# Optimization experiments

Measured on AMD Instinct MI355X. Metric: run time of the kernel, lower is better.

## Reference

```python
import jax, jax.numpy as jnp
import numpy as np

D = 128
NP_, NU_, NS_ = 50000, 100000, 20000
E_UP, E_PS, E_SU = 400000, 300000, 300000
# node type ids: 0=proxy, 1=user, 2=server
# edge types: (src_type, dst_type): (user->proxy), (proxy->server), (server->user)
EDGE_TYPES = [(1, 0), (0, 2), (2, 1)]


def _edge_index(key, e, n_src, n_dst):
    k0, k1 = jax.random.split(key)
    return jnp.stack([
        jax.random.randint(k0, (e,), 0, n_src),
        jax.random.randint(k1, (e,), 0, n_dst),
    ]).astype(jnp.int64)


def setup_inputs() -> dict:
    key = jax.random.key(0)
    ks = jax.random.split(key, 16)
    s = 0.05
    return {
        "x_proxy": jax.random.normal(ks[0], (NP_, 20), jnp.float32),
        "x_user": jax.random.normal(ks[1], (NU_, 20), jnp.float32),
        "x_server": jax.random.normal(ks[2], (NS_, 20), jnp.float32),
        "node_id_proxy": jnp.arange(NP_, dtype=jnp.int64),
        "node_id_user": jnp.arange(NU_, dtype=jnp.int64),
        "node_id_server": jnp.arange(NS_, dtype=jnp.int64),
        "ei_user_proxy": _edge_index(ks[3], E_UP, NU_, NP_),
        "ei_proxy_server": _edge_index(ks[4], E_PS, NP_, NS_),
        "ei_server_user": _edge_index(ks[5], E_SU, NS_, NU_),
        "lin_w": jax.random.normal(ks[6], (3, 20, D), jnp.float32) * s,
        "lin_b": jnp.zeros((3, D), jnp.float32),
        "emb_proxy": jax.random.normal(ks[7], (NP_, D), jnp.float32) * s,
        "emb_user": jax.random.normal(ks[8], (NU_, D), jnp.float32) * s,
        "emb_server": jax.random.normal(ks[9], (NS_, D), jnp.float32) * s,
        "qkv_w": jax.random.normal(ks[10], (2, 3, 3, D, D), jnp.float32) * s,
        "qkv_b": jnp.zeros((2, 3, 3, D), jnp.float32),
        "W_edge": jax.random.normal(ks[11], (2, 3, D, D), jnp.float32) * s,
    }


def _hetero_attention_layer(xs, qkv_w, qkv_b, W_e, edges):
    # xs: list of [N_t, D] node features per node type
    # edges: list of (src_type, dst_type, edge_index[2, E])
    outs = [jnp.zeros_like(x) for x in xs]
    scale = 1.0 / jnp.sqrt(jnp.asarray(D, jnp.float32))
    for et, (src_t, dst_t, ei) in enumerate(edges):
        q = xs[src_t] @ qkv_w[src_t, 0] + qkv_b[src_t, 0]   # [Ns, D]
        k = xs[dst_t] @ qkv_w[dst_t, 1] + qkv_b[dst_t, 1]   # [Nd, D]
        v = xs[src_t] @ qkv_w[src_t, 2] + qkv_b[src_t, 2]   # [Ns, D]
        src, dst = ei[0], ei[1]
        # per-edge score: q[src] @ W @ k[dst] / sqrt(D)
        s = jnp.einsum("ed,df,ef->e", q[src], W_e[et], k[dst]) * scale
        s = jax.nn.leaky_relu(s)
        n_dst = xs[dst_t].shape[0]
        # softmax normalized over edges sharing a destination node
        m = jax.ops.segment_max(s, dst, num_segments=n_dst)
        ex = jnp.exp(s - m[dst])
        den = jax.ops.segment_sum(ex, dst, num_segments=n_dst)
        alpha = ex / den[dst]                                # [E]
        msg = alpha[:, None] * v[src]                        # [E, D]
        outs[dst_t] = outs[dst_t] + jax.ops.segment_sum(msg, dst, num_segments=n_dst)
    return outs


def reference(x_proxy, x_user, x_server, node_id_proxy, node_id_user, node_id_server,
              ei_user_proxy, ei_proxy_server, ei_server_user,
              lin_w, lin_b, emb_proxy, emb_user, emb_server, qkv_w, qkv_b, W_edge):
    xs = [
        x_proxy @ lin_w[0] + lin_b[0] + emb_proxy[node_id_proxy],
        x_user @ lin_w[1] + lin_b[1] + emb_user[node_id_user],
        x_server @ lin_w[2] + lin_b[2] + emb_server[node_id_server],
    ]
    edges = [
        (EDGE_TYPES[0][0], EDGE_TYPES[0][1], ei_user_proxy),
        (EDGE_TYPES[1][0], EDGE_TYPES[1][1], ei_proxy_server),
        (EDGE_TYPES[2][0], EDGE_TYPES[2][1], ei_server_user),
    ]
    xs = _hetero_attention_layer(xs, qkv_w[0], qkv_b[0], W_edge[0], edges)
    xs = [jax.nn.relu(x) for x in xs]
    xs = _hetero_attention_layer(xs, qkv_w[1], qkv_b[1], W_edge[1], edges)
    # concatenate per-type outputs [proxy; user; server] -> [(NP+NU+NS), D]
    return jnp.concatenate(xs, axis=0)
```

## Files before the change

### kernel.cpp

```cpp
#include <hip/hip_runtime.h>

#define NP 50000
#define NU 100000
#define NS 20000
#define NTOT 170000
#define E0 400000
#define E1 300000
#define E2 300000

typedef _Float16 f16;
typedef __attribute__((ext_vector_type(8))) _Float16 half8;
typedef __attribute__((ext_vector_type(4))) _Float16 half4;
typedef __attribute__((ext_vector_type(4))) float f32x4;
typedef unsigned int uint32;

__global__ __launch_bounds__(256) void k_init_all(
    const float* __restrict__ xp, const float* __restrict__ xu,
    const float* __restrict__ xs, const int* __restrict__ nidp,
    const int* __restrict__ nidu, const int* __restrict__ nids,
    const float* __restrict__ lin_w, const float* __restrict__ lin_b,
    const float* __restrict__ embp, const float* __restrict__ embu,
    const float* __restrict__ embs, f16* __restrict__ xb) {
  int tid = threadIdx.x;
  int node = blockIdx.x * 8 + (tid >> 5);
  int dg = tid & 31;
  int t, local;
  const float* x;
  const int* nid;
  const float* emb;
  if (node < NP) { t = 0; local = node; x = xp; nid = nidp; emb = embp; }
  else if (node < NP + NU) { t = 1; local = node - NP; x = xu; nid = nidu; emb = embu; }
  else { t = 2; local = node - NP - NU; x = xs; nid = nids; emb = embs; }
  const float* lw = lin_w + t * 20 * 128;
  int d = dg * 4;
  float xv = (dg < 20) ? x[local * 20 + dg] : 0.f;
  float4 s = *(const float4*)&emb[(size_t)nid[local] * 128 + d];
  float4 b = *(const float4*)&lin_b[t * 128 + d];
  s.x += b.x; s.y += b.y; s.z += b.z; s.w += b.w;
#pragma unroll
  for (int j = 0; j < 20; ++j) {
    float xj = __shfl(xv, j, 32);
    float4 w = *(const float4*)&lw[j * 128 + d];
    s.x += xj * w.x; s.y += xj * w.y; s.z += xj * w.z; s.w += xj * w.w;
  }
  half4 o;
  o[0] = (f16)s.x; o[1] = (f16)s.y; o[2] = (f16)s.z; o[3] = (f16)s.w;
  *(half4*)(xb + (size_t)node * 128 + d) = o;
}

__global__ __launch_bounds__(128) void k_keff(const float* __restrict__ qkv_w,
                                              const float* __restrict__ qkv_b,
                                              const float* __restrict__ W_edge,
                                              float* __restrict__ Keff,
                                              float* __restrict__ bkeff) {
  int y = blockIdx.y;
  int l = y / 3, t = y - l * 3;
  int et = (t == 0) ? 0 : (t == 1) ? 2 : 1;
  const float* Wk = qkv_w + (size_t)(y * 3 + 1) * 16384;
  const float* bk = qkv_b + (size_t)(y * 3 + 1) * 128;
  const float* We = W_edge + (size_t)(l * 3 + et) * 16384;
  float* Ko = Keff + (size_t)y * 16384;
  float* bo = bkeff + (size_t)y * 128;

  __shared__ float Wes[128][65];
  int c = blockIdx.x, tid = threadIdx.x;
  float s = 0.f, tb = 0.f;
  for (int f0 = 0; f0 < 128; f0 += 64) {
    __syncthreads();
    int fr = tid & 63, r0 = tid >> 6;
    for (int it = 0; it < 64; ++it) {
      int row = it * 2 + r0;
      Wes[row][fr] = We[row * 128 + f0 + fr];
    }
    __syncthreads();
#pragma unroll 16
    for (int fp = 0; fp < 64; ++fp) s += Wk[c * 128 + f0 + fp] * Wes[tid][fp];
    if (c == 0) {
      for (int fp = 0; fp < 64; ++fp) tb += bk[f0 + fp] * Wes[tid][fp];
    }
  }
  Ko[c * 128 + tid] = s;
  if (c == 0) bo[tid] = tb;
}

__global__ __launch_bounds__(256) void k_splitw18(const float* __restrict__ qkv_w,
                                                  const float* __restrict__ Keff6,
                                                  f16* __restrict__ hi,
                                                  f16* __restrict__ lo) {
  int slot = blockIdx.y;
  int y = slot / 3, r = slot - y * 3;
  const float* src = (r == 1) ? (Keff6 + (size_t)y * 16384)
                              : (qkv_w + (size_t)(y * 3 + ((r == 0) ? 0 : 2)) * 16384);
  f16* h = hi + (size_t)slot * 16384;
  f16* l = lo + (size_t)slot * 16384;
  int idx = blockIdx.x * 256 + threadIdx.x;
  int n = idx >> 7, c = idx & 127;
  float f = src[c * 128 + n];
  f16 hb = (f16)f;
  h[idx] = hb;
  l[idx] = (f16)(f - (float)hb);
}

#define GB0 782
#define GB1 1563
#define GB2 313
__global__ __launch_bounds__(256, 4) void k_gemm3(
    const f16* __restrict__ Xin,
    const f16* __restrict__ WtHi, const f16* __restrict__ WtLo,
    const float* __restrict__ qkv_b, const float* __restrict__ bkeff6,
    f16* __restrict__ QV, f16* __restrict__ Kb, int l) {
  __shared__ f16 As[64 * 128];
  __shared__ f16 Ys[64 * 128];
  int bid = blockIdx.x;
  int t, row0, M, moff;
  if (bid < GB0) { t = 0; row0 = bid * 64; M = NP; moff = 0; }
  else if (bid < GB0 + GB1) { t = 1; row0 = (bid - GB0) * 64; M = NU; moff = NP; }
  else { t = 2; row0 = (bid - GB0 - GB1) * 64; M = NS; moff = NP + NU; }
  int y = l * 3 + t;
  const f16* A = Xin + (size_t)moff * 128;
  const f16* Whi = WtHi + (size_t)y * 3 * 16384;
  const f16* Wlo = WtLo + (size_t)y * 3 * 16384;

  int tid = threadIdx.x;
  int wave = tid >> 6, lane = tid & 63;
  int colw = wave * 32;
  int lrow = lane & 15, kgrp = lane >> 4;

#pragma unroll
  for (int i = 0; i < 4; ++i) {
    int chunkLin = i * 256 + tid;
    int row = chunkLin >> 4;
    int chunk = chunkLin & 15;
    int grow = row0 + row;
    if (grow >= M) grow = M - 1;
    half8 v = *(const half8*)(A + (size_t)grow * 128 + chunk * 8);
    *(half8*)(As + row * 128 + (chunk ^ (row & 7)) * 8) = v;
  }
  __syncthreads();

  int x7 = lrow & 7;

  for (int bw = 0; bw < 3; ++bw) {
    f32x4 acc[4][2] = {};
#pragma unroll
    for (int s = 0; s < 4; ++s) {
      half8 bh[2], bl[2];
#pragma unroll
      for (int nt = 0; nt < 2; ++nt) {
        int col = colw + nt * 16 + lrow;
        size_t boff = (size_t)bw * 16384 + col * 128 + s * 32 + kgrp * 8;
        bh[nt] = *(const half8*)(Whi + boff);
        bl[nt] = *(const half8*)(Wlo + boff);
      }
      int c2 = (s * 4 + kgrp) ^ x7;
#pragma unroll
      for (int mt = 0; mt < 4; ++mt) {
        int row = mt * 16 + lrow;
        half8 a = *(const half8*)(As + row * 128 + c2 * 8);
        acc[mt][0] = __builtin_amdgcn_mfma_f32_16x16x32_f16(a, bh[0], acc[mt][0], 0, 0, 0);
        acc[mt][0] = __builtin_amdgcn_mfma_f32_16x16x32_f16(a, bl[0], acc[mt][0], 0, 0, 0);
        acc[mt][1] = __builtin_amdgcn_mfma_f32_16x16x32_f16(a, bh[1], acc[mt][1], 0, 0, 0);
        acc[mt][1] = __builtin_amdgcn_mfma_f32_16x16x32_f16(a, bl[1], acc[mt][1], 0, 0, 0);
      }
    }
    const float* bias = (bw == 0) ? (qkv_b + (size_t)(y * 3 + 0) * 128)
                      : (bw == 1) ? (bkeff6 + (size_t)y * 128)
                                  : (qkv_b + (size_t)(y * 3 + 2) * 128);
    f16* Ybase = (bw == 1) ? Kb : (QV + ((bw == 2) ? 128 : 0));
    int RS = (bw == 1) ? 128 : 256;
    float b0 = bias[colw + lrow];
    float b1 = bias[colw + 16 + lrow];
    int col0i = colw + lrow;
    int col1i = colw + 16 + lrow;
    __syncthreads();
#pragma unroll
    for (int mt = 0; mt < 4; ++mt) {
#pragma unroll
      for (int r = 0; r < 4; ++r) {
        int lr = mt * 16 + kgrp * 4 + r;
        int sw = lr & 7;
        Ys[lr * 128 + (((col0i >> 3) ^ sw) * 8) + (col0i & 7)] = (f16)(acc[mt][0][r] + b0);
        Ys[lr * 128 + (((col1i >> 3) ^ sw) * 8) + (col1i & 7)] = (f16)(acc[mt][1][r] + b1);
      }
    }
    __syncthreads();
#pragma unroll
    for (int i = 0; i < 4; ++i) {
      int chunk = i * 256 + tid;
      int row = chunk >> 4, c = chunk & 15;
      int grow = row0 + row;
      if (grow < M)
        *(half8*)(Ybase + (size_t)(moff + grow) * RS + c * 8) =
            *(const half8*)(Ys + row * 128 + ((c ^ (row & 7)) * 8));
    }
  }
}

template <int MODE>
__global__ __launch_bounds__(256) void k_edge(
    const int* __restrict__ rowptr, const int* __restrict__ srcs,
    const f16* __restrict__ QV, const f16* __restrict__ Kb,
    f16* __restrict__ obf, float* __restrict__ of, float scale) {
  int gid = blockIdx.x * 256 + threadIdx.x;
  int wid = gid >> 4;
  if (wid >= NTOT) return;
  int sub = threadIdx.x & 15;
  int dstNode, srcBase;
  if (wid < NP) { dstNode = wid; srcBase = NP; }
  else if (wid < NP + NS) { dstNode = wid + 100000; srcBase = 0; }
  else { dstNode = wid - NS; srcBase = NP + NU; }

  int s0 = rowptr[wid], s1 = rowptr[wid + 1];

  float kf[8];
  {
    half8 kh = *(const half8*)(Kb + (size_t)dstNode * 128 + sub * 8);
#pragma unroll
    for (int j = 0; j < 8; ++j) kf[j] = (float)kh[j];
  }

  float acc[8] = {};
  float dsum = 0.f;
  for (int k = s0; k < s1; ++k) {
    int src = srcBase + srcs[k];
    const f16* qv = QV + (size_t)src * 256 + sub * 8;
    half8 qh = *(const half8*)qv;
    half8 vh = *(const half8*)(qv + 128);
    float p = 0.f;
#pragma unroll
    for (int j = 0; j < 8; ++j) p = fmaf((float)qh[j], kf[j], p);
    p += __shfl_xor(p, 8, 16);
    p += __shfl_xor(p, 4, 16);
    p += __shfl_xor(p, 2, 16);
    p += __shfl_xor(p, 1, 16);
    float s = p * scale;
    s = (s > 0.f) ? s : 0.01f * s;
    float e = __expf(s);
    dsum += e;
#pragma unroll
    for (int j = 0; j < 8; ++j) acc[j] = fmaf((float)vh[j], e, acc[j]);
  }

  float inv = (s1 > s0) ? 1.f / dsum : 0.f;

  if (MODE == 0) {
    half8 o;
#pragma unroll
    for (int j = 0; j < 8; ++j) o[j] = (f16)fmaxf(acc[j] * inv, 0.f);
    *(half8*)(obf + (size_t)dstNode * 128 + sub * 8) = o;
  } else {
    float4 w0, w1;
    w0.x = acc[0] * inv; w0.y = acc[1] * inv; w0.z = acc[2] * inv; w0.w = acc[3] * inv;
    w1.x = acc[4] * inv; w1.y = acc[5] * inv; w1.z = acc[6] * inv; w1.w = acc[7] * inv;
    float* orow = of + (size_t)dstNode * 128 + sub * 8;
    *(float4*)orow = w0;
    *(float4*)(orow + 4) = w1;
  }
}

__global__ void k_count_all(const int* __restrict__ e0, const int* __restrict__ e1,
                            const int* __restrict__ e2, int* __restrict__ cnt) {
  int e = blockIdx.x * 256 + threadIdx.x;
  if (e < E0) atomicAdd(&cnt[e0[E0 + e]], 1);
  else if (e < E0 + E1) atomicAdd(&cnt[NP + e1[E1 + (e - E0)]], 1);
  else if (e < E0 + E1 + E2) atomicAdd(&cnt[NP + NS + e2[E2 + (e - E0 - E1)]], 1);
}

__global__ void k_fill_all(const int* __restrict__ e0, const int* __restrict__ e1,
                           const int* __restrict__ e2, const int* __restrict__ rowptr,
                           int* __restrict__ cur, int* __restrict__ srcs) {
  int e = blockIdx.x * 256 + threadIdx.x;
  int row, src;
  if (e < E0) { row = e0[E0 + e]; src = e0[e]; }
  else if (e < E0 + E1) { row = NP + e1[E1 + (e - E0)]; src = e1[e - E0]; }
  else if (e < E0 + E1 + E2) { row = NP + NS + e2[E2 + (e - E0 - E1)]; src = e2[e - E0 - E1]; }
  else return;
  int p = atomicAdd(&cur[row], 1);
  srcs[rowptr[row] + p] = src;
}

__global__ __launch_bounds__(256) void k_blocksum(const int* __restrict__ c, int N,
                                                  int* __restrict__ bs) {
  int base = blockIdx.x * 1024;
  int t = threadIdx.x;
  int s = 0;
#pragma unroll
  for (int j = 0; j < 4; ++j) {
    int i = base + t * 4 + j;
    if (i < N) s += c[i];
  }
#pragma unroll
  for (int off = 32; off; off >>= 1) s += __shfl_down(s, off, 64);
  __shared__ int wsm[4];
  if ((t & 63) == 0) wsm[t >> 6] = s;
  __syncthreads();
  if (t == 0) bs[blockIdx.x] = wsm[0] + wsm[1] + wsm[2] + wsm[3];
}

__global__ __launch_bounds__(256) void k_scan_bsums(int* __restrict__ bs, int nb) {
  __shared__ int sm[256];
  int t = threadIdx.x;
  int v[4];
  int s = 0;
#pragma unroll
  for (int j = 0; j < 4; ++j) {
    int i = t * 4 + j;
    v[j] = (i < nb) ? bs[i] : 0;
    s += v[j];
  }
  sm[t] = s;
  __syncthreads();
  for (int off = 1; off < 256; off <<= 1) {
    int x = (t >= off) ? sm[t - off] : 0;
    __syncthreads();
    sm[t] += x;
    __syncthreads();
  }
  int run = t ? sm[t - 1] : 0;
#pragma unroll
  for (int j = 0; j < 4; ++j) {
    int i = t * 4 + j;
    if (i < nb) {
      int tmp = v[j];
      bs[i] = run;
      run += tmp;
    }
  }
}

__global__ __launch_bounds__(256) void k_scan_apply(const int* __restrict__ c,
                                                    const int* __restrict__ bofs,
                                                    int* __restrict__ rowptr, int N) {
  __shared__ int sm[256];
  int base = blockIdx.x * 1024, t = threadIdx.x;
  int v[4];
  int s = 0;
#pragma unroll
  for (int j = 0; j < 4; ++j) {
    int i = base + t * 4 + j;
    v[j] = (i < N) ? c[i] : 0;
    s += v[j];
  }
  sm[t] = s;
  __syncthreads();
  for (int off = 1; off < 256; off <<= 1) {
    int x = (t >= off) ? sm[t - off] : 0;
    __syncthreads();
    sm[t] += x;
    __syncthreads();
  }
  int run = bofs[blockIdx.x] + (t ? sm[t - 1] : 0);
#pragma unroll
  for (int j = 0; j < 4; ++j) {
    int i = base + t * 4 + j;
    if (i < N) {
      run += v[j];
      rowptr[i + 1] = run;
    }
  }
  if (blockIdx.x == 0 && t == 0) rowptr[0] = 0;
}


extern "C" void kernel_launch(void* const* d_in, const int* in_sizes, int n_in,
                              void* d_out, int out_size, void* d_ws, size_t ws_size,
                              hipStream_t stream) {
  const float* x_in[3] = {(const float*)d_in[0], (const float*)d_in[1], (const float*)d_in[2]};
  const int* nid[3] = {(const int*)d_in[3], (const int*)d_in[4], (const int*)d_in[5]};
  const int* ei[3] = {(const int*)d_in[6], (const int*)d_in[7], (const int*)d_in[8]};
  const float* lin_w = (const float*)d_in[9];
  const float* lin_b = (const float*)d_in[10];
  const float* emb[3] = {(const float*)d_in[11], (const float*)d_in[12], (const float*)d_in[13]};
  const float* qkv_w = (const float*)d_in[14];
  const float* qkv_b = (const float*)d_in[15];
  const float* W_edge = (const float*)d_in[16];
  float* out = (float*)d_out;

  char* ws = (char*)d_ws;
  size_t o = 0;
  auto carve = [&](size_t bytes) {
    char* p = ws + o;
    o = (o + bytes + 255) & ~(size_t)255;
    return p;
  };
  f16* XsA = (f16*)carve((size_t)NTOT * 128 * 2);
  f16* XsB = (f16*)carve((size_t)NTOT * 128 * 2);
  f16* QV = (f16*)carve((size_t)NTOT * 256 * 2);
  f16* Kb = (f16*)carve((size_t)NTOT * 128 * 2);
  float* Keff6 = (float*)carve((size_t)6 * 16384 * 4);
  float* bkeff6 = (float*)carve(6 * 128 * 4);
  f16* WtHi = (f16*)carve((size_t)18 * 16384 * 2);
  f16* WtLo = (f16*)carve((size_t)18 * 16384 * 2);
  int* cnt = (int*)carve((size_t)2 * NTOT * 4);
  int* cur = cnt + NTOT;
  int* bsums = (int*)carve(1024 * 4);
  int* rowptr = (int*)carve((NTOT + 1) * 4);
  int* srcs = (int*)carve((size_t)(E0 + E1 + E2) * 4);
  (void)ws_size;

  k_init_all<<<NTOT / 8, 256, 0, stream>>>(x_in[0], x_in[1], x_in[2], nid[0], nid[1],
                                           nid[2], lin_w, lin_b, emb[0], emb[1], emb[2],
                                           XsA);

  {
    const int ETOT = E0 + E1 + E2;
    int nb = (NTOT + 1023) / 1024;
    hipMemsetAsync(cnt, 0, (size_t)2 * NTOT * 4, stream);
    k_count_all<<<(ETOT + 255) / 256, 256, 0, stream>>>(ei[0], ei[1], ei[2], cnt);
    k_blocksum<<<nb, 256, 0, stream>>>(cnt, NTOT, bsums);
    k_scan_bsums<<<1, 256, 0, stream>>>(bsums, nb);
    k_scan_apply<<<nb, 256, 0, stream>>>(cnt, bsums, rowptr, NTOT);
    k_fill_all<<<(ETOT + 255) / 256, 256, 0, stream>>>(ei[0], ei[1], ei[2], rowptr, cur,
                                                       srcs);
  }

  {
    dim3 gk(128, 6);
    k_keff<<<gk, 128, 0, stream>>>(qkv_w, qkv_b, W_edge, Keff6, bkeff6);
    dim3 gs(64, 18);
    k_splitw18<<<gs, 256, 0, stream>>>(qkv_w, Keff6, WtHi, WtLo);
  }

  const float scale = 0.08838834764831845f;
  const int GEMM_BLKS = GB0 + GB1 + GB2;
  const int EDGE_BLKS = (NTOT * 16 + 255) / 256;

  for (int l = 0; l < 2; ++l) {
    const f16* Xin = (l == 0) ? XsA : XsB;
    k_gemm3<<<GEMM_BLKS, 256, 0, stream>>>(Xin, WtHi, WtLo, qkv_b, bkeff6, QV, Kb, l);
    if (l == 0)
      k_edge<0><<<EDGE_BLKS, 256, 0, stream>>>(rowptr, srcs, QV, Kb, XsB,
                                               (float*)nullptr, scale);
    else
      k_edge<1><<<EDGE_BLKS, 256, 0, stream>>>(rowptr, srcs, QV, Kb,
                                               (f16*)nullptr, out, scale);
  }
}
```

Baseline: 505.5 us.

## Tile input projection per block and prefetch next edge's Q/V in attention loop

```diff
diff --git a/kernel.cpp b/kernel.cpp
--- a/kernel.cpp
+++ b/kernel.cpp
@@ -14,6 +14,9 @@
 typedef __attribute__((ext_vector_type(4))) float f32x4;
 typedef unsigned int uint32;
 
+#define IB0 782
+#define IB1 1563
+#define IB2 313
 __global__ __launch_bounds__(256) void k_init_all(
     const float* __restrict__ xp, const float* __restrict__ xu,
     const float* __restrict__ xs, const int* __restrict__ nidp,
@@ -21,31 +24,53 @@
     const float* __restrict__ lin_w, const float* __restrict__ lin_b,
     const float* __restrict__ embp, const float* __restrict__ embu,
     const float* __restrict__ embs, f16* __restrict__ xb) {
-  int tid = threadIdx.x;
-  int node = blockIdx.x * 8 + (tid >> 5);
-  int dg = tid & 31;
-  int t, local;
+  __shared__ float xl[64 * 20];
+  int bid = blockIdx.x, tid = threadIdx.x;
+  int t, base, M, goff;
   const float* x;
   const int* nid;
   const float* emb;
-  if (node < NP) { t = 0; local = node; x = xp; nid = nidp; emb = embp; }
-  else if (node < NP + NU) { t = 1; local = node - NP; x = xu; nid = nidu; emb = embu; }
-  else { t = 2; local = node - NP - NU; x = xs; nid = nids; emb = embs; }
-  const float* lw = lin_w + t * 20 * 128;
+  if (bid < IB0) { t = 0; base = bid * 64; M = NP; goff = 0; x = xp; nid = nidp; emb = embp; }
+  else if (bid < IB0 + IB1) { t = 1; base = (bid - IB0) * 64; M = NU; goff = NP; x = xu; nid = nidu; emb = embu; }
+  else { t = 2; base = (bid - IB0 - IB1) * 64; M = NS; goff = NP + NU; x = xs; nid = nids; emb = embs; }
+
+#pragma unroll
+  for (int i = 0; i < 5; ++i) {
+    int idx = i * 256 + tid;
+    int nn = idx / 20, jj = idx - nn * 20;
+    int gn = base + nn;
+    if (gn >= M) gn = M - 1;
+    xl[idx] = x[gn * 20 + jj];
+  }
+  __syncthreads();
+
+  int dg = tid & 31, ns = tid >> 5;
   int d = dg * 4;
-  float xv = (dg < 20) ? x[local * 20 + dg] : 0.f;
-  float4 s = *(const float4*)&emb[(size_t)nid[local] * 128 + d];
-  float4 b = *(const float4*)&lin_b[t * 128 + d];
-  s.x += b.x; s.y += b.y; s.z += b.z; s.w += b.w;
-#pragma unroll
-  for (int j = 0; j < 20; ++j) {
-    float xj = __shfl(xv, j, 32);
-    float4 w = *(const float4*)&lw[j * 128 + d];
-    s.x += xj * w.x; s.y += xj * w.y; s.z += xj * w.z; s.w += xj * w.w;
-  }
-  half4 o;
-  o[0] = (f16)s.x; o[1] = (f16)s.y; o[2] = (f16)s.z; o[3] = (f16)s.w;
-  *(half4*)(xb + (size_t)node * 128 + d) = o;
+  const float* lw = lin_w + t * 20 * 128 + d;
+  float4 w[20];
+#pragma unroll
+  for (int j = 0; j < 20; ++j) w[j] = *(const float4*)(lw + j * 128);
+  float4 bb = *(const float4*)&lin_b[t * 128 + d];
+
+#pragma unroll 2
+  for (int i = 0; i < 8; ++i) {
+    int ln = i * 8 + ns;
+    int gn = base + ln;
+    bool ok = gn < M;
+    int gnc = ok ? gn : M - 1;
+    float4 s = *(const float4*)&emb[(size_t)nid[gnc] * 128 + d];
+    s.x += bb.x; s.y += bb.y; s.z += bb.z; s.w += bb.w;
+#pragma unroll
+    for (int j = 0; j < 20; ++j) {
+      float xj = xl[ln * 20 + j];
+      s.x += xj * w[j].x; s.y += xj * w[j].y; s.z += xj * w[j].z; s.w += xj * w[j].w;
+    }
+    if (ok) {
+      half4 o;
+      o[0] = (f16)s.x; o[1] = (f16)s.y; o[2] = (f16)s.z; o[3] = (f16)s.w;
+      *(half4*)(xb + (size_t)(goff + gn) * 128 + d) = o;
+    }
+  }
 }
 
 __global__ __launch_bounds__(128) void k_keff(const float* __restrict__ qkv_w,
@@ -221,11 +246,21 @@
 
   float acc[8] = {};
   float dsum = 0.f;
-  for (int k = s0; k < s1; ++k) {
-    int src = srcBase + srcs[k];
-    const f16* qv = QV + (size_t)src * 256 + sub * 8;
-    half8 qh = *(const half8*)qv;
-    half8 vh = *(const half8*)(qv + 128);
+  int k = s0;
+  half8 qN, vN;
+  if (k < s1) {
+    const f16* qv = QV + (size_t)(srcBase + srcs[k]) * 256 + sub * 8;
+    qN = *(const half8*)qv;
+    vN = *(const half8*)(qv + 128);
+  }
+  while (k < s1) {
+    half8 qh = qN, vh = vN;
+    int kn = k + 1;
+    if (kn < s1) {
+      const f16* qv = QV + (size_t)(srcBase + srcs[kn]) * 256 + sub * 8;
+      qN = *(const half8*)qv;
+      vN = *(const half8*)(qv + 128);
+    }
     float p = 0.f;
 #pragma unroll
     for (int j = 0; j < 8; ++j) p = fmaf((float)qh[j], kf[j], p);
@@ -239,6 +274,7 @@
     dsum += e;
 #pragma unroll
     for (int j = 0; j < 8; ++j) acc[j] = fmaf((float)vh[j], e, acc[j]);
+    k = kn;
   }
 
   float inv = (s1 > s0) ? 1.f / dsum : 0.f;
@@ -398,9 +434,9 @@
   int* srcs = (int*)carve((size_t)(E0 + E1 + E2) * 4);
   (void)ws_size;
 
-  k_init_all<<<NTOT / 8, 256, 0, stream>>>(x_in[0], x_in[1], x_in[2], nid[0], nid[1],
-                                           nid[2], lin_w, lin_b, emb[0], emb[1], emb[2],
-                                           XsA);
+  k_init_all<<<IB0 + IB1 + IB2, 256, 0, stream>>>(
+      x_in[0], x_in[1], x_in[2], nid[0], nid[1], nid[2], lin_w, lin_b, emb[0],
+      emb[1], emb[2], XsA);
 
   {
     const int ETOT = E0 + E1 + E2;
```

Result: faster. 472.4 us (-6.5%).
